# Optimization experiments

Measured on AMD Instinct MI355X. Metric: run time of the kernel, lower is better.

## Reference

```python
import jax, jax.numpy as jnp
from jax import lax
import numpy as np

T, B, D, H = 1024, 512, 128, 128  # time steps, batch, input dim, hidden size


def setup_inputs() -> dict:
    key = jax.random.key(0)
    ks = jax.random.split(key, 8)
    s_fc = 1.0 / np.sqrt(D)
    s_gru = 1.0 / np.sqrt(H)
    return {
        "x": jax.random.normal(ks[0], (T, B, D), dtype=jnp.float32),
        "W1": jax.random.uniform(ks[1], (128, D), jnp.float32, -s_fc, s_fc),
        "b1": jax.random.uniform(ks[2], (128,), jnp.float32, -s_fc, s_fc),
        "W_ih": jax.random.uniform(ks[3], (3 * H, 128), jnp.float32, -s_gru, s_gru),
        "W_hh": jax.random.uniform(ks[4], (3 * H, H), jnp.float32, -s_gru, s_gru),
        "b_ih": jax.random.uniform(ks[5], (3 * H,), jnp.float32, -s_gru, s_gru),
        "b_hh": jax.random.uniform(ks[6], (3 * H,), jnp.float32, -s_gru, s_gru),
    }


def reference(x, W1, b1, W_ih, W_hh, b_ih, b_hh):
    # fc1 applied to every step (batched once over T*B for efficiency)
    feats = jnp.einsum('tbd,hd->tbh', x, W1) + b1  # [T, B, 128]

    hidden = W_hh.shape[1]

    def step(h, f):
        # PyTorch GRUCell gate math
        gi = f @ W_ih.T + b_ih          # [B, 3H]
        gh = h @ W_hh.T + b_hh          # [B, 3H]
        i_r, i_z, i_n = jnp.split(gi, 3, axis=-1)
        h_r, h_z, h_n = jnp.split(gh, 3, axis=-1)
        r = jax.nn.sigmoid(i_r + h_r)
        z = jax.nn.sigmoid(i_z + h_z)
        n = jnp.tanh(i_n + r * h_n)
        h_new = (1.0 - z) * n + z * h
        return h_new, None

    # first call gru(feats) passes no hidden -> zeros initial state
    h0 = jnp.zeros((x.shape[1], hidden), dtype=x.dtype)
    h_final, _ = lax.scan(step, h0, feats)
    return h_final  # [B, H]
```

## Files before the change

kernel.cpp:

```cpp
#include <hip/hip_runtime.h>
#include <hip/hip_bf16.h>

#define T_STEPS 1024
#define BATCH   512
#define DIM     128
#define G3      384
#define NCHUNK  (T_STEPS/8)
#define GI_STRIDE 129

typedef __attribute__((ext_vector_type(8))) short bf16x8;
typedef __attribute__((ext_vector_type(4))) float f32x4;

#define LOG2E  1.44269504f
#define LOG2E2 2.88539008f
#define NV_CLAMP 43.28f

__device__ __forceinline__ short f2bf(float f) {
  unsigned u = __builtin_bit_cast(unsigned, f);
  u += 0x7FFFu + ((u >> 16) & 1u);
  return (short)(u >> 16);
}

__device__ __forceinline__ void block_sync_lds() {
  asm volatile("s_waitcnt lgkmcnt(0)\n\ts_barrier" ::: "memory");
}

__global__ void prep_kernel(const float* __restrict__ W1, const float* __restrict__ b1,
                            const float* __restrict__ W_ih, const float* __restrict__ W_hh,
                            const float* __restrict__ b_ih, const float* __restrict__ b_hh,
                            short* __restrict__ wc_bf, short* __restrict__ whh_bf,
                            float* __restrict__ bc, float* __restrict__ bhh_s) {
  const int g = blockIdx.x;
  const int d = threadIdx.x;
  const float sg = (g < 256) ? LOG2E : LOG2E2;
  float acc = 0.f;
  #pragma unroll 4
  for (int k = 0; k < 128; ++k)
    acc = fmaf(W_ih[g * 128 + k], W1[k * 128 + d], acc);
  wc_bf[g * 128 + d]  = f2bf(acc * sg);
  whh_bf[g * 128 + d] = f2bf(W_hh[g * 128 + d] * sg);

  __shared__ float red[128];
  red[d] = W_ih[g * 128 + d] * b1[d];
  __syncthreads();
  #pragma unroll
  for (int s = 64; s > 0; s >>= 1) {
    if (d < s) red[d] += red[d + s];
    __syncthreads();
  }
  if (d == 0) {
    bc[g]    = (red[0] + b_ih[g]) * sg;
    bhh_s[g] = b_hh[g] * sg;
  }
}

__global__ __launch_bounds__(512, 2) void gru_kernel(
    const float* __restrict__ x,
    const float* __restrict__ bhh_s,
    const short* __restrict__ wc_bf,
    const short* __restrict__ whh_bf,
    const float* __restrict__ bc,
    float* __restrict__ out)
{
  const int tid = threadIdx.x;
  const int w   = tid >> 6;
  const int l   = tid & 63;
  const int q   = l >> 4;
  const int c   = l & 15;
  const int b0  = blockIdx.x * 2;

  __shared__ f32x4 gi4[2 * 16 * GI_STRIDE];
  __shared__ short hbuf[2][2][128];

  const f32x4 zero4 = {0.f, 0.f, 0.f, 0.f};

  if (w < 4) {
    const int half = q & 1;
    const int ch   = q >> 1;
    const int colX = w * 32 + (half << 4) + c;

    bf16x8 Bh[3][2][4];
    #pragma unroll
    for (int g = 0; g < 3; ++g)
      #pragma unroll
      for (int Tt = 0; Tt < 2; ++Tt)
        #pragma unroll
        for (int kt = 0; kt < 4; ++kt)
          Bh[g][Tt][kt] = *(const bf16x8*)(whh_bf +
              (g * 128 + w * 32 + Tt * 16 + c) * 128 + kt * 32 + q * 8);
    const float bhn = bhh_s[256 + colX];

    ((short*)hbuf)[tid] = 0;
    float hp = 0.f;
    __syncthreads();

    const short* hb0 = &hbuf[0][c >> 3][q * 8];
    const short* hb1 = &hbuf[1][c >> 3][q * 8];

    __builtin_amdgcn_s_setprio(1);
    for (int cc = 0; cc < NCHUNK; ++cc) {
      f32x4 gi[8];
      {
        const f32x4* gp = gi4 + (cc & 1) * (16 * GI_STRIDE) + ch * GI_STRIDE + colX;
        #pragma unroll
        for (int s = 0; s < 8; ++s) gi[s] = gp[2 * s * GI_STRIDE];
      }
      #pragma unroll
      for (int s = 0; s < 8; ++s) {
        const short* hb = (s & 1) ? hb1 : hb0;
        bf16x8 Ah[4];
        #pragma unroll
        for (int kt = 0; kt < 4; ++kt)
          Ah[kt] = *(const bf16x8*)(hb + kt * 32);

        f32x4 r0A = __builtin_amdgcn_mfma_f32_16x16x32_bf16(Ah[0], Bh[0][0][0], zero4, 0, 0, 0);
        f32x4 r1A = __builtin_amdgcn_mfma_f32_16x16x32_bf16(Ah[0], Bh[0][1][0], zero4, 0, 0, 0);
        f32x4 r0B = __builtin_amdgcn_mfma_f32_16x16x32_bf16(Ah[2], Bh[0][0][2], zero4, 0, 0, 0);
        f32x4 r1B = __builtin_amdgcn_mfma_f32_16x16x32_bf16(Ah[2], Bh[0][1][2], zero4, 0, 0, 0);
        r0A = __builtin_amdgcn_mfma_f32_16x16x32_bf16(Ah[1], Bh[0][0][1], r0A, 0, 0, 0);
        r1A = __builtin_amdgcn_mfma_f32_16x16x32_bf16(Ah[1], Bh[0][1][1], r1A, 0, 0, 0);
        r0B = __builtin_amdgcn_mfma_f32_16x16x32_bf16(Ah[3], Bh[0][0][3], r0B, 0, 0, 0);
        r1B = __builtin_amdgcn_mfma_f32_16x16x32_bf16(Ah[3], Bh[0][1][3], r1B, 0, 0, 0);
        f32x4 z0A = __builtin_amdgcn_mfma_f32_16x16x32_bf16(Ah[0], Bh[1][0][0], zero4, 0, 0, 0);
        f32x4 z1A = __builtin_amdgcn_mfma_f32_16x16x32_bf16(Ah[0], Bh[1][1][0], zero4, 0, 0, 0);
        f32x4 z0B = __builtin_amdgcn_mfma_f32_16x16x32_bf16(Ah[2], Bh[1][0][2], zero4, 0, 0, 0);
        f32x4 z1B = __builtin_amdgcn_mfma_f32_16x16x32_bf16(Ah[2], Bh[1][1][2], zero4, 0, 0, 0);
        z0A = __builtin_amdgcn_mfma_f32_16x16x32_bf16(Ah[1], Bh[1][0][1], z0A, 0, 0, 0);
        z1A = __builtin_amdgcn_mfma_f32_16x16x32_bf16(Ah[1], Bh[1][1][1], z1A, 0, 0, 0);
        z0B = __builtin_amdgcn_mfma_f32_16x16x32_bf16(Ah[3], Bh[1][0][3], z0B, 0, 0, 0);
        z1B = __builtin_amdgcn_mfma_f32_16x16x32_bf16(Ah[3], Bh[1][1][3], z1B, 0, 0, 0);

        const float ghr = half ? (r1A[0] + r1B[0]) : (r0A[0] + r0B[0]);
        const float ghz = half ? (z1A[0] + z1B[0]) : (z0A[0] + z0B[0]);
        const float rg = __builtin_amdgcn_rcpf(1.f + __builtin_amdgcn_exp2f(-(gi[s][0] + ghr)));
        const float zg = __builtin_amdgcn_rcpf(1.f + __builtin_amdgcn_exp2f(-(gi[s][1] + ghz)));

        f32x4 n0A = __builtin_amdgcn_mfma_f32_16x16x32_bf16(Ah[0], Bh[2][0][0], zero4, 0, 0, 0);
        f32x4 n1A = __builtin_amdgcn_mfma_f32_16x16x32_bf16(Ah[0], Bh[2][1][0], zero4, 0, 0, 0);
        f32x4 n0B = __builtin_amdgcn_mfma_f32_16x16x32_bf16(Ah[2], Bh[2][0][2], zero4, 0, 0, 0);
        f32x4 n1B = __builtin_amdgcn_mfma_f32_16x16x32_bf16(Ah[2], Bh[2][1][2], zero4, 0, 0, 0);
        n0A = __builtin_amdgcn_mfma_f32_16x16x32_bf16(Ah[1], Bh[2][0][1], n0A, 0, 0, 0);
        n1A = __builtin_amdgcn_mfma_f32_16x16x32_bf16(Ah[1], Bh[2][1][1], n1A, 0, 0, 0);
        n0B = __builtin_amdgcn_mfma_f32_16x16x32_bf16(Ah[3], Bh[2][0][3], n0B, 0, 0, 0);
        n1B = __builtin_amdgcn_mfma_f32_16x16x32_bf16(Ah[3], Bh[2][1][3], n1B, 0, 0, 0);
        const float ghn = half ? (n1A[0] + n1B[0]) : (n0A[0] + n0B[0]);

        float nv = gi[s][2] + rg * (ghn + bhn);
        nv = fminf(fmaxf(nv, -NV_CLAMP), NV_CLAMP);
        const float e  = __builtin_amdgcn_exp2f(nv);
        const float nn = 1.f - 2.f * __builtin_amdgcn_rcpf(e + 1.f);
        const float h  = zg * (hp - nn) + nn;
        hp = h;
        hbuf[(s & 1) ^ 1][ch][colX] = f2bf(h);
        block_sync_lds();
      }
    }
    __builtin_amdgcn_s_setprio(0);
    out[(size_t)(b0 + ch) * DIM + colX] = hp;
  } else {
    const int w4 = w - 4;
    const int jg0 = w4 * 32 + c, jg1 = jg0 + 16;
    bf16x8 Bc[3][2][4];
    #pragma unroll
    for (int g = 0; g < 3; ++g)
      #pragma unroll
      for (int Tt = 0; Tt < 2; ++Tt)
        #pragma unroll
        for (int kt = 0; kt < 4; ++kt)
          Bc[g][Tt][kt] = *(const bf16x8*)(wc_bf +
              (g * 128 + w4 * 32 + Tt * 16 + c) * 128 + kt * 32 + q * 8);
    const float fr0 = bc[jg0]       + bhh_s[jg0];
    const float fz0 = bc[128 + jg0] + bhh_s[128 + jg0];
    const float fn0 = bc[256 + jg0];
    const float fr1 = bc[jg1]       + bhh_s[jg1];
    const float fz1 = bc[128 + jg1] + bhh_s[128 + jg1];
    const float fn1 = bc[256 + jg1];

    const int trel = c >> 1, chn = c & 1;
    f32x4 xv[8];

    {
      const float* xb = x + ((size_t)trel * BATCH + (b0 + chn)) * DIM + q * 8;
      f32x4 xt[8];
      #pragma unroll
      for (int kt = 0; kt < 4; ++kt) {
        xt[2 * kt]     = *(const f32x4*)(xb + kt * 32);
        xt[2 * kt + 1] = *(const f32x4*)(xb + kt * 32 + 4);
      }
      bf16x8 Ax[4];
      #pragma unroll
      for (int kt = 0; kt < 4; ++kt) {
        const f32x4 v0 = xt[2 * kt], v1 = xt[2 * kt + 1];
        bf16x8 a;
        a[0] = f2bf(v0[0]); a[1] = f2bf(v0[1]); a[2] = f2bf(v0[2]); a[3] = f2bf(v0[3]);
        a[4] = f2bf(v1[0]); a[5] = f2bf(v1[1]); a[6] = f2bf(v1[2]); a[7] = f2bf(v1[3]);
        Ax[kt] = a;
      }
      f32x4 ga[2][3];
      #pragma unroll
      for (int g = 0; g < 3; ++g) {
        ga[0][g] = __builtin_amdgcn_mfma_f32_16x16x32_bf16(Ax[0], Bc[g][0][0], zero4, 0, 0, 0);
        ga[1][g] = __builtin_amdgcn_mfma_f32_16x16x32_bf16(Ax[0], Bc[g][1][0], zero4, 0, 0, 0);
      }
      #pragma unroll
      for (int kt = 1; kt < 4; ++kt)
        #pragma unroll
        for (int g = 0; g < 3; ++g) {
          ga[0][g] = __builtin_amdgcn_mfma_f32_16x16x32_bf16(Ax[kt], Bc[g][0][kt], ga[0][g], 0, 0, 0);
          ga[1][g] = __builtin_amdgcn_mfma_f32_16x16x32_bf16(Ax[kt], Bc[g][1][kt], ga[1][g], 0, 0, 0);
        }
      #pragma unroll
      for (int r = 0; r < 4; ++r) {
        f32x4 vA = {ga[0][0][r] + fr0, ga[0][1][r] + fz0, ga[0][2][r] + fn0, 0.f};
        f32x4 vB = {ga[1][0][r] + fr1, ga[1][1][r] + fz1, ga[1][2][r] + fn1, 0.f};
        gi4[(4 * q + r) * GI_STRIDE + jg0] = vA;
        gi4[(4 * q + r) * GI_STRIDE + jg1] = vB;
      }
      const float* xb1 = x + ((size_t)(8 + trel) * BATCH + (b0 + chn)) * DIM + q * 8;
      #pragma unroll
      for (int kt = 0; kt < 4; ++kt) {
        xv[2 * kt]     = *(const f32x4*)(xb1 + kt * 32);
        xv[2 * kt + 1] = *(const f32x4*)(xb1 + kt * 32 + 4);
      }
    }
    __syncthreads();

    for (int cc = 0; cc < NCHUNK; ++cc) {
      const int tc = cc + 1;
      bf16x8 Ax[4];
      f32x4 ga[2][3];
      #pragma unroll
      for (int s = 0; s < 8; ++s) {
        if (tc < NCHUNK) {
          if (s == 0) {
            #pragma unroll
            for (int kt = 0; kt < 4; ++kt) {
              const f32x4 v0 = xv[2 * kt], v1 = xv[2 * kt + 1];
              bf16x8 a;
              a[0] = f2bf(v0[0]); a[1] = f2bf(v0[1]); a[2] = f2bf(v0[2]); a[3] = f2bf(v0[3]);
              a[4] = f2bf(v1[0]); a[5] = f2bf(v1[1]); a[6] = f2bf(v1[2]); a[7] = f2bf(v1[3]);
              Ax[kt] = a;
            }
          } else if (s == 1) {
            #pragma unroll
            for (int g = 0; g < 3; ++g) {
              ga[0][g] = __builtin_amdgcn_mfma_f32_16x16x32_bf16(Ax[0], Bc[g][0][0], zero4, 0, 0, 0);
              ga[1][g] = __builtin_amdgcn_mfma_f32_16x16x32_bf16(Ax[0], Bc[g][1][0], zero4, 0, 0, 0);
            }
          } else if (s <= 4) {
            const int kt = s - 1;
            #pragma unroll
            for (int g = 0; g < 3; ++g) {
              ga[0][g] = __builtin_amdgcn_mfma_f32_16x16x32_bf16(Ax[kt], Bc[g][0][kt], ga[0][g], 0, 0, 0);
              ga[1][g] = __builtin_amdgcn_mfma_f32_16x16x32_bf16(Ax[kt], Bc[g][1][kt], ga[1][g], 0, 0, 0);
            }
          } else if (s == 5) {
            if (tc + 1 < NCHUNK) {
              const float* xb = x + ((size_t)((tc + 1) * 8 + trel) * BATCH + (b0 + chn)) * DIM + q * 8;
              #pragma unroll
              for (int kt = 0; kt < 4; ++kt) {
                xv[2 * kt]     = *(const f32x4*)(xb + kt * 32);
                xv[2 * kt + 1] = *(const f32x4*)(xb + kt * 32 + 4);
              }
            }
          } else if (s == 6) {
            #pragma unroll
            for (int r = 0; r < 4; ++r) {
              ga[0][0][r] += fr0; ga[0][1][r] += fz0; ga[0][2][r] += fn0;
              ga[1][0][r] += fr1; ga[1][1][r] += fz1; ga[1][2][r] += fn1;
            }
          } else {
            f32x4* gb = gi4 + (tc & 1) * (16 * GI_STRIDE);
            #pragma unroll
            for (int r = 0; r < 4; ++r) {
              f32x4 vA = {ga[0][0][r], ga[0][1][r], ga[0][2][r], 0.f};
              f32x4 vB = {ga[1][0][r], ga[1][1][r], ga[1][2][r], 0.f};
              gb[(4 * q + r) * GI_STRIDE + jg0] = vA;
              gb[(4 * q + r) * GI_STRIDE + jg1] = vB;
            }
          }
        }
        block_sync_lds();
      }
    }
  }
}

extern "C" void kernel_launch(void* const* d_in, const int* in_sizes, int n_in,
                              void* d_out, int out_size, void* d_ws, size_t ws_size,
                              hipStream_t stream) {
  const float* x    = (const float*)d_in[0];
  const float* W1   = (const float*)d_in[1];
  const float* b1   = (const float*)d_in[2];
  const float* W_ih = (const float*)d_in[3];
  const float* W_hh = (const float*)d_in[4];
  const float* b_ih = (const float*)d_in[5];
  const float* b_hh = (const float*)d_in[6];
  float* out = (float*)d_out;

  char* ws = (char*)d_ws;
  short* wc_bf  = (short*)(ws);
  short* whh_bf = (short*)(ws + 98304);
  float* bc     = (float*)(ws + 196608);
  float* bhh_s  = (float*)(ws + 198144);

  prep_kernel<<<dim3(G3), dim3(128), 0, stream>>>(W1, b1, W_ih, W_hh, b_ih, b_hh,
                                                  wc_bf, whh_bf, bc, bhh_s);
  gru_kernel<<<dim3(BATCH / 2), dim3(512), 0, stream>>>(x, bhh_s, wc_bf, whh_bf, bc, out);
}
```

Baseline: 680.9 us.

## Rebalance producer MFMA schedule, prefetch gate inputs per step, pad hidden buffer

The recurrent warps now load each step's input-gate vector one step ahead instead of loading all eight at the start of a chunk, which lowers register pressure. The r/z sigmoids move after all MFMAs are issued, the nv clamp is removed, and the update uses fmaf. The gi LDS layout drops its padding stride, while the hidden-state buffer gains a padded row stride. The producer warps spread their 24 MFMAs evenly over six sub-steps and fold the bias add into the store. Dropping the clamp relies on exp2 saturating correctly, and the unpadded gi layout may bring LDS bank conflicts back.

```diff
diff --git a/kernel.cpp b/kernel.cpp
--- a/kernel.cpp
+++ b/kernel.cpp
@@ -6,14 +6,14 @@
 #define DIM     128
 #define G3      384
 #define NCHUNK  (T_STEPS/8)
-#define GI_STRIDE 129
 
 typedef __attribute__((ext_vector_type(8))) short bf16x8;
 typedef __attribute__((ext_vector_type(4))) float f32x4;
 
 #define LOG2E  1.44269504f
 #define LOG2E2 2.88539008f
-#define NV_CLAMP 43.28f
+
+#define HSTRIDE 160
 
 __device__ __forceinline__ short f2bf(float f) {
   unsigned u = __builtin_bit_cast(unsigned, f);
@@ -69,8 +69,8 @@
   const int c   = l & 15;
   const int b0  = blockIdx.x * 2;
 
-  __shared__ f32x4 gi4[2 * 16 * GI_STRIDE];
-  __shared__ short hbuf[2][2][128];
+  __shared__ f32x4 gi4[2][16][128];
+  __shared__ short hbuf[2][2][HSTRIDE];
 
   const f32x4 zero4 = {0.f, 0.f, 0.f, 0.f};
 
@@ -91,6 +91,7 @@
     const float bhn = bhh_s[256 + colX];
 
     ((short*)hbuf)[tid] = 0;
+    if (tid < 2 * HSTRIDE - 256) ((short*)hbuf)[256 + tid] = 0;
     float hp = 0.f;
     __syncthreads();
 
@@ -99,12 +100,8 @@
 
     __builtin_amdgcn_s_setprio(1);
     for (int cc = 0; cc < NCHUNK; ++cc) {
-      f32x4 gi[8];
-      {
-        const f32x4* gp = gi4 + (cc & 1) * (16 * GI_STRIDE) + ch * GI_STRIDE + colX;
-        #pragma unroll
-        for (int s = 0; s < 8; ++s) gi[s] = gp[2 * s * GI_STRIDE];
-      }
+      const f32x4* gp = &gi4[cc & 1][ch][colX];
+      f32x4 gcur = gp[0];
       #pragma unroll
       for (int s = 0; s < 8; ++s) {
         const short* hb = (s & 1) ? hb1 : hb0;
@@ -112,6 +109,8 @@
         #pragma unroll
         for (int kt = 0; kt < 4; ++kt)
           Ah[kt] = *(const bf16x8*)(hb + kt * 32);
+        f32x4 gnext = zero4;
+        if (s < 7) gnext = gp[2 * (s + 1) * 128];
 
         f32x4 r0A = __builtin_amdgcn_mfma_f32_16x16x32_bf16(Ah[0], Bh[0][0][0], zero4, 0, 0, 0);
         f32x4 r1A = __builtin_amdgcn_mfma_f32_16x16x32_bf16(Ah[0], Bh[0][1][0], zero4, 0, 0, 0);
@@ -129,12 +128,6 @@
         z1A = __builtin_amdgcn_mfma_f32_16x16x32_bf16(Ah[1], Bh[1][1][1], z1A, 0, 0, 0);
         z0B = __builtin_amdgcn_mfma_f32_16x16x32_bf16(Ah[3], Bh[1][0][3], z0B, 0, 0, 0);
         z1B = __builtin_amdgcn_mfma_f32_16x16x32_bf16(Ah[3], Bh[1][1][3], z1B, 0, 0, 0);
-
-        const float ghr = half ? (r1A[0] + r1B[0]) : (r0A[0] + r0B[0]);
-        const float ghz = half ? (z1A[0] + z1B[0]) : (z0A[0] + z0B[0]);
-        const float rg = __builtin_amdgcn_rcpf(1.f + __builtin_amdgcn_exp2f(-(gi[s][0] + ghr)));
-        const float zg = __builtin_amdgcn_rcpf(1.f + __builtin_amdgcn_exp2f(-(gi[s][1] + ghz)));
-
         f32x4 n0A = __builtin_amdgcn_mfma_f32_16x16x32_bf16(Ah[0], Bh[2][0][0], zero4, 0, 0, 0);
         f32x4 n1A = __builtin_amdgcn_mfma_f32_16x16x32_bf16(Ah[0], Bh[2][1][0], zero4, 0, 0, 0);
         f32x4 n0B = __builtin_amdgcn_mfma_f32_16x16x32_bf16(Ah[2], Bh[2][0][2], zero4, 0, 0, 0);
@@ -143,15 +136,19 @@
         n1A = __builtin_amdgcn_mfma_f32_16x16x32_bf16(Ah[1], Bh[2][1][1], n1A, 0, 0, 0);
         n0B = __builtin_amdgcn_mfma_f32_16x16x32_bf16(Ah[3], Bh[2][0][3], n0B, 0, 0, 0);
         n1B = __builtin_amdgcn_mfma_f32_16x16x32_bf16(Ah[3], Bh[2][1][3], n1B, 0, 0, 0);
+
+        const float ghr = half ? (r1A[0] + r1B[0]) : (r0A[0] + r0B[0]);
+        const float ghz = half ? (z1A[0] + z1B[0]) : (z0A[0] + z0B[0]);
+        const float rg = __builtin_amdgcn_rcpf(1.f + __builtin_amdgcn_exp2f(-(gcur[0] + ghr)));
+        const float zg = __builtin_amdgcn_rcpf(1.f + __builtin_amdgcn_exp2f(-(gcur[1] + ghz)));
         const float ghn = half ? (n1A[0] + n1B[0]) : (n0A[0] + n0B[0]);
-
-        float nv = gi[s][2] + rg * (ghn + bhn);
-        nv = fminf(fmaxf(nv, -NV_CLAMP), NV_CLAMP);
+        const float nv = fmaf(rg, ghn + bhn, gcur[2]);
         const float e  = __builtin_amdgcn_exp2f(nv);
         const float nn = 1.f - 2.f * __builtin_amdgcn_rcpf(e + 1.f);
-        const float h  = zg * (hp - nn) + nn;
+        const float h  = fmaf(zg, hp - nn, nn);
         hp = h;
         hbuf[(s & 1) ^ 1][ch][colX] = f2bf(h);
+        gcur = gnext;
         block_sync_lds();
       }
     }
@@ -213,8 +210,8 @@
       for (int r = 0; r < 4; ++r) {
         f32x4 vA = {ga[0][0][r] + fr0, ga[0][1][r] + fz0, ga[0][2][r] + fn0, 0.f};
         f32x4 vB = {ga[1][0][r] + fr1, ga[1][1][r] + fz1, ga[1][2][r] + fn1, 0.f};
-        gi4[(4 * q + r) * GI_STRIDE + jg0] = vA;
-        gi4[(4 * q + r) * GI_STRIDE + jg1] = vB;
+        gi4[0][4 * q + r][jg0] = vA;
+        gi4[0][4 * q + r][jg1] = vB;
       }
       const float* xb1 = x + ((size_t)(8 + trel) * BATCH + (b0 + chn)) * DIM + q * 8;
       #pragma unroll
@@ -241,21 +238,20 @@
               a[4] = f2bf(v1[0]); a[5] = f2bf(v1[1]); a[6] = f2bf(v1[2]); a[7] = f2bf(v1[3]);
               Ax[kt] = a;
             }
-          } else if (s == 1) {
+          } else if (s <= 6) {
             #pragma unroll
-            for (int g = 0; g < 3; ++g) {
-              ga[0][g] = __builtin_amdgcn_mfma_f32_16x16x32_bf16(Ax[0], Bc[g][0][0], zero4, 0, 0, 0);
-              ga[1][g] = __builtin_amdgcn_mfma_f32_16x16x32_bf16(Ax[0], Bc[g][1][0], zero4, 0, 0, 0);
+            for (int uu = 0; uu < 2; ++uu) {
+              const int u = 2 * (s - 1) + uu;
+              const int kt = u / 3, g = u % 3;
+              if (kt == 0) {
+                ga[0][g] = __builtin_amdgcn_mfma_f32_16x16x32_bf16(Ax[0], Bc[g][0][0], zero4, 0, 0, 0);
+                ga[1][g] = __builtin_amdgcn_mfma_f32_16x16x32_bf16(Ax[0], Bc[g][1][0], zero4, 0, 0, 0);
+              } else {
+                ga[0][g] = __builtin_amdgcn_mfma_f32_16x16x32_bf16(Ax[kt], Bc[g][0][kt], ga[0][g], 0, 0, 0);
+                ga[1][g] = __builtin_amdgcn_mfma_f32_16x16x32_bf16(Ax[kt], Bc[g][1][kt], ga[1][g], 0, 0, 0);
+              }
             }
-          } else if (s <= 4) {
-            const int kt = s - 1;
-            #pragma unroll
-            for (int g = 0; g < 3; ++g) {
-              ga[0][g] = __builtin_amdgcn_mfma_f32_16x16x32_bf16(Ax[kt], Bc[g][0][kt], ga[0][g], 0, 0, 0);
-              ga[1][g] = __builtin_amdgcn_mfma_f32_16x16x32_bf16(Ax[kt], Bc[g][1][kt], ga[1][g], 0, 0, 0);
-            }
-          } else if (s == 5) {
-            if (tc + 1 < NCHUNK) {
+            if (s == 5 && tc + 1 < NCHUNK) {
               const float* xb = x + ((size_t)((tc + 1) * 8 + trel) * BATCH + (b0 + chn)) * DIM + q * 8;
               #pragma unroll
               for (int kt = 0; kt < 4; ++kt) {
@@ -263,20 +259,14 @@
                 xv[2 * kt + 1] = *(const f32x4*)(xb + kt * 32 + 4);
               }
             }
-          } else if (s == 6) {
+          } else {
+            const int nbuf = tc & 1;
             #pragma unroll
             for (int r = 0; r < 4; ++r) {
-              ga[0][0][r] += fr0; ga[0][1][r] += fz0; ga[0][2][r] += fn0;
-              ga[1][0][r] += fr1; ga[1][1][r] += fz1; ga[1][2][r] += fn1;
-            }
-          } else {
-            f32x4* gb = gi4 + (tc & 1) * (16 * GI_STRIDE);
-            #pragma unroll
-            for (int r = 0; r < 4; ++r) {
-              f32x4 vA = {ga[0][0][r], ga[0][1][r], ga[0][2][r], 0.f};
-              f32x4 vB = {ga[1][0][r], ga[1][1][r], ga[1][2][r], 0.f};
-              gb[(4 * q + r) * GI_STRIDE + jg0] = vA;
-              gb[(4 * q + r) * GI_STRIDE + jg1] = vB;
+              f32x4 vA = {ga[0][0][r] + fr0, ga[0][1][r] + fz0, ga[0][2][r] + fn0, 0.f};
+              f32x4 vB = {ga[1][0][r] + fr1, ga[1][1][r] + fz1, ga[1][2][r] + fn1, 0.f};
+              gi4[nbuf][4 * q + r][jg0] = vA;
+              gi4[nbuf][4 * q + r][jg1] = vB;
             }
           }
         }
```

Measured after the change: 684.2 us. Within noise of the previous version (+0.5%).
